# Kernel optimization log

Measured on AMD Instinct MI355X. Metric: run time of the kernel, lower is better.

The kernel has to match this reference:

```python
import jax, jax.numpy as jnp
import numpy as np

E, KD, VD = 1024, 1024, 1024
B, S = 4, 4096


def setup_inputs() -> dict:
    key = jax.random.key(0)
    ks = jax.random.split(key, 7)
    sE, sK = 1.0 / np.sqrt(E), 1.0 / np.sqrt(E)
    return {
        "x": jax.random.normal(ks[0], (B, S, E), dtype=jnp.float32),
        "Wq": jax.random.normal(ks[1], (E, KD), dtype=jnp.float32) * sE,
        "bq": jnp.zeros((KD,), dtype=jnp.float32),
        "Wk": jax.random.normal(ks[2], (E, KD), dtype=jnp.float32) * sE,
        "bk": jnp.zeros((KD,), dtype=jnp.float32),
        "Wv": jax.random.normal(ks[3], (E, VD), dtype=jnp.float32) * sE,
        "bv": jnp.zeros((VD,), dtype=jnp.float32),
    }


def reference(x, Wq, bq, Wk, bk, Wv, bv):
    # Separate Q/K/V projections (nn.Linear equivalents)
    Q = jnp.einsum("bse,ek->bsk", x, Wq) + bq  # [B,S,KD]
    K = jnp.einsum("bse,ek->bsk", x, Wk) + bk  # [B,S,KD]
    V = jnp.einsum("bse,ev->bsv", x, Wv) + bv  # [B,S,VD]
    scale = 1.0 / jnp.sqrt(jnp.float32(KD))
    scores = jnp.einsum("bqk,bsk->bqs", Q, K) * scale  # [B,S,S]
    attn = jax.nn.softmax(scores, axis=-1)
    out = jnp.einsum("bqs,bsv->bqv", attn, V)  # [B,S,VD]
    return out
```

## Files before the change

kernel.cpp:

```cpp
#include <hip/hip_runtime.h>
#include <cstdint>
#include <math.h>

typedef __attribute__((ext_vector_type(8))) short short8;
typedef __attribute__((ext_vector_type(4))) float f32x4;

#define AS1C const __attribute__((address_space(1))) void*
#define AS3  __attribute__((address_space(3))) void*

__device__ __forceinline__ unsigned short f2bf(float f) {
  union { float f; unsigned int u; } v; v.f = f;
  unsigned int r = v.u + 0x7FFFu + ((v.u >> 16) & 1u);
  return (unsigned short)(r >> 16);
}

__global__ void cast_x_kernel(const float* __restrict__ x, unsigned short* __restrict__ xb) {
  int i = blockIdx.x * blockDim.x + threadIdx.x;
  float4 v = ((const float4*)x)[i];
  ushort4 o;
  o.x = f2bf(v.x); o.y = f2bf(v.y); o.z = f2bf(v.z); o.w = f2bf(v.w);
  ((ushort4*)xb)[i] = o;
}

__global__ void zero_f4_kernel(float4* __restrict__ o) {
  size_t i = (size_t)blockIdx.x * blockDim.x + threadIdx.x;
  float4 z; z.x = 0.f; z.y = 0.f; z.z = 0.f; z.w = 0.f;
  o[i] = z;
}

__global__ void transpose_cast_kernel(const float* __restrict__ W0, const float* __restrict__ W1,
                                      const float* __restrict__ W2,
                                      unsigned short* __restrict__ T0, unsigned short* __restrict__ T1,
                                      unsigned short* __restrict__ T2) {
  __shared__ float tile[32][33];
  const float* W = (blockIdx.z == 0) ? W0 : (blockIdx.z == 1 ? W1 : W2);
  unsigned short* T = (blockIdx.z == 0) ? T0 : (blockIdx.z == 1 ? T1 : T2);
  int tx = threadIdx.x & 31, ty = threadIdx.x >> 5;
  int bx = blockIdx.x * 32, by = blockIdx.y * 32;
#pragma unroll
  for (int i = 0; i < 32; i += 8)
    tile[ty + i][tx] = W[(size_t)(by + ty + i) * 1024 + bx + tx];
  __syncthreads();
#pragma unroll
  for (int i = 0; i < 32; i += 8)
    T[(size_t)(bx + ty + i) * 1024 + by + tx] = f2bf(tile[tx][ty + i]);
}

template <int KDIM, int NT>
__device__ __forceinline__ void gemm_core8(const unsigned short* __restrict__ Abase,
                                           const unsigned short* __restrict__ Btbase,
                                           unsigned short* smem, f32x4 acc[8][4]) {
  const int t = threadIdx.x;
  const int lane = t & 63, wave = t >> 6;
  const int wm = wave >> 2, wn = wave & 3;
  const int quad = lane >> 4, l16 = lane & 15;

  const unsigned short* srcp[4];
  int dstoff[4];
#pragma unroll
  for (int s = 0; s < 4; ++s) {
    int gi = t + s * 512;
    int idx = gi & 1023;
    int row = idx >> 2;
    int sg = (idx & 3) ^ (row & 3);
    srcp[s] = ((gi >> 10) ? Btbase : Abase) + (size_t)row * KDIM + sg * 8;
    dstoff[s] = gi * 8;
  }

  auto stage2 = [&](int reg, int T, int h, int pair) {
    unsigned short* buf = smem + reg * 16384;
#pragma unroll
    for (int s2 = 0; s2 < 2; ++s2) {
      int s = pair * 2 + s2;
      __builtin_amdgcn_global_load_lds((AS1C)(srcp[s] + T * 64 + h * 32),
                                       (AS3)(buf + dstoff[s]), 16, 0, 0);
    }
  };
  auto rdA4 = [&](short8* a, int reg, int mb) {
    const unsigned short* buf = smem + reg * 16384;
#pragma unroll
    for (int i = 0; i < 4; ++i) {
      int row = wm * 128 + (mb + i) * 16 + l16;
      a[i] = *(const short8*)(buf + row * 32 + ((quad ^ (row & 3)) << 3));
    }
  };
  auto rdB4 = [&](short8* b, int reg) {
    const unsigned short* buf = smem + reg * 16384 + 8192;
#pragma unroll
    for (int i = 0; i < 4; ++i) {
      int row = wn * 64 + i * 16 + l16;
      b[i] = *(const short8*)(buf + row * 32 + ((quad ^ (row & 3)) << 3));
    }
  };
  auto mf16 = [&](short8* a, short8* b, int mb) {
    __builtin_amdgcn_s_setprio(1);
#pragma unroll
    for (int mi = 0; mi < 4; ++mi)
#pragma unroll
      for (int ni = 0; ni < 4; ++ni)
        acc[mb + mi][ni] =
            __builtin_amdgcn_mfma_f32_16x16x32_bf16(a[mi], b[ni], acc[mb + mi][ni], 0, 0, 0);
    __builtin_amdgcn_s_setprio(0);
  };

#define BAR()   asm volatile("s_barrier" ::: "memory")
#define LGKM0() asm volatile("s_waitcnt lgkmcnt(0)" ::: "memory")
#define VM(N)   asm volatile("s_waitcnt vmcnt(" #N ")" ::: "memory")

  stage2(0, 0, 0, 0); stage2(0, 0, 0, 1);
  stage2(1, 0, 1, 0); stage2(1, 0, 1, 1);
  stage2(2, 1, 0, 0); stage2(2, 1, 0, 1);
  VM(8);
  BAR();

  short8 a0[4], a1[4], b0[4];
  for (int it = 0; it < NT / 2; ++it) {
    const int T = 2 * it;
    const bool lastI = (it == NT / 2 - 1);
    rdA4(a0, 0, 0); rdB4(b0, 0);
    stage2(3, T + 1, 1, 0);
    BAR(); LGKM0();
    mf16(a0, b0, 0);
    BAR();
    rdA4(a1, 0, 4);
    stage2(3, T + 1, 1, 1);
    VM(8);
    BAR(); LGKM0();
    mf16(a1, b0, 4);
    BAR();
    rdA4(a0, 1, 0); rdB4(b0, 1);
    if (!lastI) stage2(0, T + 2, 0, 0);
    BAR(); LGKM0();
    mf16(a0, b0, 0);
    BAR();
    rdA4(a1, 1, 4);
    if (!lastI) { stage2(0, T + 2, 0, 1); VM(8); }
    else        { VM(4); }
    BAR(); LGKM0();
    mf16(a1, b0, 4);
    BAR();
    rdA4(a0, 2, 0); rdB4(b0, 2);
    if (!lastI) stage2(1, T + 2, 1, 0);
    BAR(); LGKM0();
    mf16(a0, b0, 0);
    BAR();
    rdA4(a1, 2, 4);
    if (!lastI) { stage2(1, T + 2, 1, 1); VM(8); }
    else        { VM(0); }
    BAR(); LGKM0();
    mf16(a1, b0, 4);
    BAR();
    rdA4(a0, 3, 0); rdB4(b0, 3);
    if (!lastI) stage2(2, T + 3, 0, 0);
    BAR(); LGKM0();
    mf16(a0, b0, 0);
    BAR();
    rdA4(a1, 3, 4);
    if (!lastI) { stage2(2, T + 3, 0, 1); VM(8); }
    BAR(); LGKM0();
    mf16(a1, b0, 4);
    BAR();
  }
#undef BAR
#undef LGKM0
#undef VM
}

struct ProjArgs {
  const unsigned short* bt[3];
  const float* bias[3];
  unsigned short* c[3];
};
struct SPairArgs {
  const unsigned short* q[2];
  const unsigned short* k[2];
  unsigned short* pc[2][4];
  float* rs[2];
};
struct PVPairArgs {
  const unsigned short* pc[2][4];
  const unsigned short* vt[2];
  const float* rs[2];
  float* out[2];
};

__global__ __launch_bounds__(512, 2) void gemm256_proj(
    const unsigned short* __restrict__ A, ProjArgs pa) {
  extern __shared__ unsigned short smem[];
  const int t = threadIdx.x;
  const int lane = t & 63, wave = t >> 6;
  const int wm = wave >> 2, wn = wave & 3;
  const int quad = lane >> 4, l16 = lane & 15;
  const int z = blockIdx.z;

  const int gx = gridDim.x;
  const int nwg = gx * gridDim.y;
  int bid = blockIdx.y * gx + blockIdx.x;
  bid = (bid & 7) * (nwg >> 3) + (bid >> 3);
  const int bx = bid % gx, by = bid / gx;
  const int m0 = bx * 256, n0 = by * 256;

  f32x4 acc[8][4];
  const f32x4 fz = {0.f, 0.f, 0.f, 0.f};
#pragma unroll
  for (int mi = 0; mi < 8; ++mi)
#pragma unroll
    for (int ni = 0; ni < 4; ++ni) acc[mi][ni] = fz;

  gemm_core8<1024, 16>(A + (size_t)m0 * 1024, pa.bt[z] + (size_t)n0 * 1024, smem, acc);

  const float* bias = pa.bias[z];
  unsigned short* C = pa.c[z];
  const float scale = (z == 0) ? 0.03125f : 1.0f;
  if (z < 2) {
#pragma unroll
    for (int mi = 0; mi < 8; ++mi) {
      int row = m0 + wm * 128 + mi * 16 + quad * 4;
#pragma unroll
      for (int ni = 0; ni < 4; ++ni) {
        int col = n0 + wn * 64 + ni * 16 + l16;
        float bv = bias[col];
#pragma unroll
        for (int r = 0; r < 4; ++r)
          C[(size_t)(row + r) * 1024 + col] = f2bf((acc[mi][ni][r] + bv) * scale);
      }
    }
  } else {
#pragma unroll
    for (int mi = 0; mi < 8; ++mi) {
      int row = m0 + wm * 128 + mi * 16 + quad * 4;
      int bb = row >> 12, ss = row & 4095;
#pragma unroll
      for (int ni = 0; ni < 4; ++ni) {
        int col = n0 + wn * 64 + ni * 16 + l16;
        float bv = bias[col];
        ushort4 pk;
        pk.x = f2bf(acc[mi][ni][0] + bv);
        pk.y = f2bf(acc[mi][ni][1] + bv);
        pk.z = f2bf(acc[mi][ni][2] + bv);
        pk.w = f2bf(acc[mi][ni][3] + bv);
        *(ushort4*)&C[((size_t)bb * 1024 + col) * 4096 + ss] = pk;
      }
    }
  }
}

__global__ __launch_bounds__(512, 2) void gemm256_s(SPairArgs sa) {
  extern __shared__ unsigned short smem[];
  const int t = threadIdx.x;
  const int lane = t & 63, wave = t >> 6;
  const int wm = wave >> 2, wn = wave & 3;
  const int quad = lane >> 4, l16 = lane & 15;
  const int z = blockIdx.z;

  const int gx = gridDim.x;
  const int nwg = gx * gridDim.y;
  int bid = blockIdx.y * gx + blockIdx.x;
  bid = (bid & 7) * (nwg >> 3) + (bid >> 3);
  const int bx = bid % gx, by = bid / gx;
  const int m0 = bx * 256, n0 = by * 256;

  f32x4 acc[8][4];
  const f32x4 fz = {0.f, 0.f, 0.f, 0.f};
#pragma unroll
  for (int mi = 0; mi < 8; ++mi)
#pragma unroll
    for (int ni = 0; ni < 4; ++ni) acc[mi][ni] = fz;

  gemm_core8<1024, 16>(sa.q[z] + (size_t)m0 * 1024, sa.k[z] + (size_t)n0 * 1024, smem, acc);

  unsigned short* base = sa.pc[z][m0 >> 10];
  float* rs = sa.rs[z];
#pragma unroll
  for (int mi = 0; mi < 8; ++mi) {
    int row = m0 + wm * 128 + mi * 16 + quad * 4;
    int rowl = row & 1023;
    float pr[4] = {0.f, 0.f, 0.f, 0.f};
#pragma unroll
    for (int ni = 0; ni < 4; ++ni) {
      int col = n0 + wn * 64 + ni * 16 + l16;
#pragma unroll
      for (int r = 0; r < 4; ++r) {
        float p = __expf(acc[mi][ni][r]);
        base[(size_t)(rowl + r) * 4096 + col] = f2bf(p);
        pr[r] += p;
      }
    }
#pragma unroll
    for (int r = 0; r < 4; ++r) {
      float v = pr[r];
      v += __shfl_xor(v, 1);
      v += __shfl_xor(v, 2);
      v += __shfl_xor(v, 4);
      v += __shfl_xor(v, 8);
      if (l16 == 0) atomicAdd(&rs[row + r], v);
    }
  }
}

__global__ __launch_bounds__(512, 2) void gemm256_pv(PVPairArgs va) {
  extern __shared__ unsigned short smem[];
  const int t = threadIdx.x;
  const int lane = t & 63, wave = t >> 6;
  const int wm = wave >> 2, wn = wave & 3;
  const int quad = lane >> 4, l16 = lane & 15;
  const int z = blockIdx.z;

  const int gx = gridDim.x, gy = gridDim.y;
  const int nwg = gx * gy;
  int lid = blockIdx.y * gx + blockIdx.x;
  int s = (lid & 7) * (nwg >> 3) + (lid >> 3);
  const int bx = s / gy, by = s % gy;
  const int m0 = bx * 256, n0 = by * 256;

  f32x4 acc[8][4];
  const f32x4 fz = {0.f, 0.f, 0.f, 0.f};
#pragma unroll
  for (int mi = 0; mi < 8; ++mi)
#pragma unroll
    for (int ni = 0; ni < 4; ++ni) acc[mi][ni] = fz;

  const unsigned short* Abase = va.pc[z][m0 >> 10] + (size_t)(m0 & 1023) * 4096;
  gemm_core8<4096, 64>(Abase, va.vt[z] + (size_t)n0 * 4096, smem, acc);

  const float* rs = va.rs[z];
  float* outp = va.out[z];
#pragma unroll
  for (int mi = 0; mi < 8; ++mi) {
    int row = m0 + wm * 128 + mi * 16 + quad * 4;
    float inv[4];
#pragma unroll
    for (int r = 0; r < 4; ++r) inv[r] = 1.0f / rs[row + r];
#pragma unroll
    for (int ni = 0; ni < 4; ++ni) {
      int col = n0 + wn * 64 + ni * 16 + l16;
#pragma unroll
      for (int r = 0; r < 4; ++r)
        outp[(size_t)(row + r) * 1024 + col] = acc[mi][ni][r] * inv[r];
    }
  }
}

extern "C" void kernel_launch(void* const* d_in, const int* in_sizes, int n_in,
                              void* d_out, int out_size, void* d_ws, size_t ws_size,
                              hipStream_t stream) {
  const float* x  = (const float*)d_in[0];
  const float* Wq = (const float*)d_in[1];
  const float* bq = (const float*)d_in[2];
  const float* Wk = (const float*)d_in[3];
  const float* bk = (const float*)d_in[4];
  const float* Wv = (const float*)d_in[5];
  const float* bv = (const float*)d_in[6];
  float* out = (float*)d_out;

  const size_t MR = (size_t)16384 * 1024;
  const size_t SB = (size_t)4096 * 1024;
  unsigned short* xb  = (unsigned short*)d_ws;
  unsigned short* Qb  = xb + MR;
  unsigned short* Kb  = Qb + MR;
  unsigned short* Vtb = Kb + MR;
  unsigned short* WqT = Vtb + MR;
  unsigned short* WkT = WqT + (size_t)1024 * 1024;
  unsigned short* WvT = WkT + (size_t)1024 * 1024;
  float* rs = (float*)WqT;
  unsigned short* outU = (unsigned short*)(out + (size_t)2 * 4096 * 1024);

  hipFuncSetAttribute((const void*)gemm256_proj,
                      hipFuncAttributeMaxDynamicSharedMemorySize, 131072);
  hipFuncSetAttribute((const void*)gemm256_s,
                      hipFuncAttributeMaxDynamicSharedMemorySize, 131072);
  hipFuncSetAttribute((const void*)gemm256_pv,
                      hipFuncAttributeMaxDynamicSharedMemorySize, 131072);

  cast_x_kernel<<<16384, 256, 0, stream>>>(x, xb);
  transpose_cast_kernel<<<dim3(32, 32, 3), 256, 0, stream>>>(Wq, Wk, Wv, WqT, WkT, WvT);

  ProjArgs pa;
  pa.bt[0] = WqT;  pa.bt[1] = WkT;  pa.bt[2] = WvT;
  pa.bias[0] = bq; pa.bias[1] = bk; pa.bias[2] = bv;
  pa.c[0] = Qb;    pa.c[1] = Kb;    pa.c[2] = Vtb;
  gemm256_proj<<<dim3(64, 4, 3), 512, 131072, stream>>>(xb, pa);

  zero_f4_kernel<<<16, 256, 0, stream>>>((float4*)rs);

  SPairArgs sA;
  sA.q[0] = Qb;      sA.k[0] = Kb;      sA.rs[0] = rs;
  sA.q[1] = Qb + SB; sA.k[1] = Kb + SB; sA.rs[1] = rs + 4096;
  for (int c = 0; c < 4; ++c) { sA.pc[0][c] = xb + (size_t)c * SB; sA.pc[1][c] = outU + (size_t)c * SB; }
  gemm256_s<<<dim3(16, 16, 2), 512, 131072, stream>>>(sA);

  PVPairArgs vA;
  for (int c = 0; c < 4; ++c) { vA.pc[0][c] = sA.pc[0][c]; vA.pc[1][c] = sA.pc[1][c]; }
  vA.vt[0] = Vtb;      vA.rs[0] = rs;        vA.out[0] = out;
  vA.vt[1] = Vtb + SB; vA.rs[1] = rs + 4096; vA.out[1] = out + (size_t)4096 * 1024;
  gemm256_pv<<<dim3(16, 4, 2), 512, 131072, stream>>>(vA);

  SPairArgs sB;
  sB.q[0] = Qb + 2 * SB; sB.k[0] = Kb + 2 * SB; sB.rs[0] = rs + 2 * 4096;
  sB.q[1] = Qb + 3 * SB; sB.k[1] = Kb + 3 * SB; sB.rs[1] = rs + 3 * 4096;
  for (int c = 0; c < 4; ++c) sB.pc[0][c] = xb + (size_t)c * SB;
  sB.pc[1][0] = Qb; sB.pc[1][1] = Qb + SB; sB.pc[1][2] = Kb; sB.pc[1][3] = Kb + SB;
  gemm256_s<<<dim3(16, 16, 2), 512, 131072, stream>>>(sB);

  PVPairArgs vB;
  for (int c = 0; c < 4; ++c) { vB.pc[0][c] = sB.pc[0][c]; vB.pc[1][c] = sB.pc[1][c]; }
  vB.vt[0] = Vtb + 2 * SB; vB.rs[0] = rs + 2 * 4096; vB.out[0] = out + (size_t)2 * 4096 * 1024;
  vB.vt[1] = Vtb + 3 * SB; vB.rs[1] = rs + 3 * 4096; vB.out[1] = out + (size_t)3 * 4096 * 1024;
  gemm256_pv<<<dim3(16, 4, 2), 512, 131072, stream>>>(vB);
}
```

Baseline: 628.3 us.

## Interleave A and B tiles per LDS row with 8-way XOR swizzle

Changes the shared-memory staging layout in the GEMM core. Each LDS row now holds 64 bf16, the first half an A row and the second half the matching B row, with an 8-way XOR swizzle in place of 4-way. Each thread loads from a single base pointer and advances by 32-element k-chunks, so NT doubles and the pipelined loop steps four k-chunks per iteration. The goal is cheaper address generation, fewer live source pointers and fewer LDS bank conflicts on the fragment reads. The cost is a riskier indexing scheme that must stay consistent with the staging pipeline.

```diff
diff --git a/kernel.cpp b/kernel.cpp
--- a/kernel.cpp
+++ b/kernel.cpp
@@ -55,25 +55,20 @@
   const int wm = wave >> 2, wn = wave & 3;
   const int quad = lane >> 4, l16 = lane & 15;
 
-  const unsigned short* srcp[4];
-  int dstoff[4];
-#pragma unroll
-  for (int s = 0; s < 4; ++s) {
-    int gi = t + s * 512;
-    int idx = gi & 1023;
-    int row = idx >> 2;
-    int sg = (idx & 3) ^ (row & 3);
-    srcp[s] = ((gi >> 10) ? Btbase : Abase) + (size_t)row * KDIM + sg * 8;
-    dstoff[s] = gi * 8;
-  }
-
-  auto stage2 = [&](int reg, int T, int h, int pair) {
+  const int row0 = t >> 3;
+  const int gsw = (t & 7) ^ (row0 & 7);
+  const unsigned short* gsrc =
+      (gsw & 4) ? (Btbase + (size_t)row0 * KDIM + (size_t)(gsw - 4) * 8)
+                : (Abase + (size_t)row0 * KDIM + (size_t)gsw * 8);
+
+  auto stage2 = [&](int reg, int T, int pair) {
     unsigned short* buf = smem + reg * 16384;
-#pragma unroll
-    for (int s2 = 0; s2 < 2; ++s2) {
-      int s = pair * 2 + s2;
-      __builtin_amdgcn_global_load_lds((AS1C)(srcp[s] + T * 64 + h * 32),
-                                       (AS3)(buf + dstoff[s]), 16, 0, 0);
+    const unsigned short* s = gsrc + T * 32;
+#pragma unroll
+    for (int j2 = 0; j2 < 2; ++j2) {
+      int j = pair * 2 + j2;
+      __builtin_amdgcn_global_load_lds((AS1C)(s + (size_t)j * 64 * KDIM),
+                                       (AS3)(buf + (t + j * 512) * 8), 16, 0, 0);
     }
   };
   auto rdA4 = [&](short8* a, int reg, int mb) {
@@ -81,15 +76,15 @@
 #pragma unroll
     for (int i = 0; i < 4; ++i) {
       int row = wm * 128 + (mb + i) * 16 + l16;
-      a[i] = *(const short8*)(buf + row * 32 + ((quad ^ (row & 3)) << 3));
+      a[i] = *(const short8*)(buf + row * 64 + ((quad ^ (row & 7)) << 3));
     }
   };
   auto rdB4 = [&](short8* b, int reg) {
-    const unsigned short* buf = smem + reg * 16384 + 8192;
+    const unsigned short* buf = smem + reg * 16384;
 #pragma unroll
     for (int i = 0; i < 4; ++i) {
       int row = wn * 64 + i * 16 + l16;
-      b[i] = *(const short8*)(buf + row * 32 + ((quad ^ (row & 3)) << 3));
+      b[i] = *(const short8*)(buf + row * 64 + (((4 + quad) ^ (row & 7)) << 3));
     }
   };
   auto mf16 = [&](short8* a, short8* b, int mb) {
@@ -107,56 +102,56 @@
 #define LGKM0() asm volatile("s_waitcnt lgkmcnt(0)" ::: "memory")
 #define VM(N)   asm volatile("s_waitcnt vmcnt(" #N ")" ::: "memory")
 
-  stage2(0, 0, 0, 0); stage2(0, 0, 0, 1);
-  stage2(1, 0, 1, 0); stage2(1, 0, 1, 1);
-  stage2(2, 1, 0, 0); stage2(2, 1, 0, 1);
+  stage2(0, 0, 0); stage2(0, 0, 1);
+  stage2(1, 1, 0); stage2(1, 1, 1);
+  stage2(2, 2, 0); stage2(2, 2, 1);
   VM(8);
   BAR();
 
   short8 a0[4], a1[4], b0[4];
-  for (int it = 0; it < NT / 2; ++it) {
-    const int T = 2 * it;
-    const bool lastI = (it == NT / 2 - 1);
+  for (int it = 0; it < NT / 4; ++it) {
+    const int T = 4 * it;
+    const bool lastI = (it == NT / 4 - 1);
     rdA4(a0, 0, 0); rdB4(b0, 0);
-    stage2(3, T + 1, 1, 0);
+    stage2(3, T + 3, 0);
     BAR(); LGKM0();
     mf16(a0, b0, 0);
     BAR();
     rdA4(a1, 0, 4);
-    stage2(3, T + 1, 1, 1);
+    stage2(3, T + 3, 1);
     VM(8);
     BAR(); LGKM0();
     mf16(a1, b0, 4);
     BAR();
     rdA4(a0, 1, 0); rdB4(b0, 1);
-    if (!lastI) stage2(0, T + 2, 0, 0);
+    if (!lastI) stage2(0, T + 4, 0);
     BAR(); LGKM0();
     mf16(a0, b0, 0);
     BAR();
     rdA4(a1, 1, 4);
-    if (!lastI) { stage2(0, T + 2, 0, 1); VM(8); }
+    if (!lastI) { stage2(0, T + 4, 1); VM(8); }
     else        { VM(4); }
     BAR(); LGKM0();
     mf16(a1, b0, 4);
     BAR();
     rdA4(a0, 2, 0); rdB4(b0, 2);
-    if (!lastI) stage2(1, T + 2, 1, 0);
+    if (!lastI) stage2(1, T + 5, 0);
     BAR(); LGKM0();
     mf16(a0, b0, 0);
     BAR();
     rdA4(a1, 2, 4);
-    if (!lastI) { stage2(1, T + 2, 1, 1); VM(8); }
+    if (!lastI) { stage2(1, T + 5, 1); VM(8); }
     else        { VM(0); }
     BAR(); LGKM0();
     mf16(a1, b0, 4);
     BAR();
     rdA4(a0, 3, 0); rdB4(b0, 3);
-    if (!lastI) stage2(2, T + 3, 0, 0);
+    if (!lastI) stage2(2, T + 6, 0);
     BAR(); LGKM0();
     mf16(a0, b0, 0);
     BAR();
     rdA4(a1, 3, 4);
-    if (!lastI) { stage2(2, T + 3, 0, 1); VM(8); }
+    if (!lastI) { stage2(2, T + 6, 1); VM(8); }
     BAR(); LGKM0();
     mf16(a1, b0, 4);
     BAR();
@@ -207,7 +202,7 @@
 #pragma unroll
     for (int ni = 0; ni < 4; ++ni) acc[mi][ni] = fz;
 
-  gemm_core8<1024, 16>(A + (size_t)m0 * 1024, pa.bt[z] + (size_t)n0 * 1024, smem, acc);
+  gemm_core8<1024, 32>(A + (size_t)m0 * 1024, pa.bt[z] + (size_t)n0 * 1024, smem, acc);
 
   const float* bias = pa.bias[z];
   unsigned short* C = pa.c[z];
@@ -267,7 +262,7 @@
 #pragma unroll
     for (int ni = 0; ni < 4; ++ni) acc[mi][ni] = fz;
 
-  gemm_core8<1024, 16>(sa.q[z] + (size_t)m0 * 1024, sa.k[z] + (size_t)n0 * 1024, smem, acc);
+  gemm_core8<1024, 32>(sa.q[z] + (size_t)m0 * 1024, sa.k[z] + (size_t)n0 * 1024, smem, acc);
 
   unsigned short* base = sa.pc[z][m0 >> 10];
   float* rs = sa.rs[z];
@@ -321,7 +316,7 @@
     for (int ni = 0; ni < 4; ++ni) acc[mi][ni] = fz;
 
   const unsigned short* Abase = va.pc[z][m0 >> 10] + (size_t)(m0 & 1023) * 4096;
-  gemm_core8<4096, 64>(Abase, va.vt[z] + (size_t)n0 * 4096, smem, acc);
+  gemm_core8<4096, 128>(Abase, va.vt[z] + (size_t)n0 * 4096, smem, acc);
 
   const float* rs = va.rs[z];
   float* outp = va.out[z];
```

Result: faster. 578.7 us (-7.9%).
